# Performance work log

Measured on AMD Instinct MI355X. Metric: run time of the kernel, lower is better.

Reference implementation:

```python
import jax, jax.numpy as jnp
import numpy as np
from jax.scipy.special import erf, erfc

N_ATOMS = 4096
BOX_L = 60.0
CUTOFF = 9.0
GRID = (64, 64, 64)
ORDER = 4
ALPHA = 0.34
COULOMB = 138.935456


def _bspline_weights(t, order):
    # Cardinal B-spline recursion (OpenMM/NNPOps convention).
    # w[..., j] = M_order(t + order - 1 - j), t in [0, 1)
    w = jnp.zeros(t.shape + (order,), t.dtype)
    w = w.at[..., 0].set(1.0 - t)
    w = w.at[..., 1].set(t)
    for k in range(3, order + 1):
        div = 1.0 / (k - 1)
        new = jnp.zeros_like(w)
        new = new.at[..., k - 1].set(div * t * w[..., k - 2])
        for j in range(1, k - 1):
            new = new.at[..., k - 1 - j].set(
                div * ((t + j) * w[..., k - 2 - j] + (k - j - t) * w[..., k - 1 - j]))
        new = new.at[..., 0].set(div * (1.0 - t) * w[..., 0])
        w = new
    return w


def _bspline_moduli(K, order):
    # |b(m)|^2 = 1 / |sum_k M_n(k+1) exp(2 pi i m k / K)|^2
    w = _bspline_weights(jnp.zeros((), jnp.float32), order)  # w[j] = M_n(n-1-j)
    mvals = w[::-1][1:]                                      # M_n(1), ..., M_n(n-1)
    data = jnp.zeros((K,), jnp.float32).at[jnp.arange(order - 1)].set(mvals)
    d2 = jnp.abs(jnp.fft.fft(data)) ** 2
    return 1.0 / jnp.maximum(d2, 1e-7)


def _min_image(delta, box, inv_box):
    s = delta @ inv_box
    s = s - jnp.round(s)
    return s @ box


def _pme_energy(positions, charges, box_vectors, exclusions):
    N = positions.shape[0]
    Kx, Ky, Kz = GRID
    inv_box = jnp.linalg.inv(box_vectors)

    # ---------------- direct space: erfc-screened pairwise sum with cutoff & exclusions
    delta = positions[:, None, :] - positions[None, :, :]          # [N,N,3]
    delta = _min_image(delta, box_vectors, inv_box)
    r2 = jnp.sum(delta * delta, axis=-1)                           # [N,N]
    rows = jnp.broadcast_to(jnp.arange(N)[:, None], exclusions.shape)
    excl_cols = jnp.where(exclusions >= 0, exclusions, rows)       # map padding -1 -> self
    excl_mask = jnp.zeros((N, N), bool).at[rows, excl_cols].set(True)
    pair_mask = jnp.triu(jnp.ones((N, N), bool), 1) & (r2 < CUTOFF ** 2) & (~excl_mask)
    r = jnp.sqrt(jnp.where(pair_mask, r2, 1.0))
    qq = charges[:, None] * charges[None, :]
    edir = COULOMB * jnp.sum(jnp.where(pair_mask, qq * erfc(ALPHA * r) / r, 0.0))

    # ---------------- reciprocal space: B-spline spread -> FFT -> influence function
    frac = positions @ inv_box
    frac = frac - jnp.floor(frac)                                  # wrap into [0,1)
    u = frac * jnp.asarray(GRID, frac.dtype)                       # [N,3] grid coords
    base = jnp.floor(u).astype(jnp.int32)
    t = u - jnp.floor(u)
    wx = _bspline_weights(t[:, 0], ORDER)                          # [N,order]
    wy = _bspline_weights(t[:, 1], ORDER)
    wz = _bspline_weights(t[:, 2], ORDER)
    offs = jnp.arange(ORDER, dtype=jnp.int32) - (ORDER - 1)        # weight j -> floor(u)-n+1+j
    ix = (base[:, 0:1] + offs) % Kx
    iy = (base[:, 1:2] + offs) % Ky
    iz = (base[:, 2:3] + offs) % Kz
    vals = (charges[:, None, None, None] * wx[:, :, None, None]
            * wy[:, None, :, None] * wz[:, None, None, :])         # [N,n,n,n]
    flat = (ix[:, :, None, None] * Ky + iy[:, None, :, None]) * Kz + iz[:, None, None, :]
    grid = jnp.zeros(Kx * Ky * Kz, positions.dtype).at[flat.reshape(-1)].add(
        vals.reshape(-1)).reshape(GRID)

    Fq = jnp.fft.fftn(grid)
    mx = (jnp.fft.fftfreq(Kx) * Kx).astype(positions.dtype)
    my = (jnp.fft.fftfreq(Ky) * Ky).astype(positions.dtype)
    mz = (jnp.fft.fftfreq(Kz) * Kz).astype(positions.dtype)
    m = jnp.stack(jnp.meshgrid(mx, my, mz, indexing='ij'), axis=-1)  # [Kx,Ky,Kz,3]
    kvec = m @ inv_box.T                                             # reciprocal vectors
    msq = jnp.sum(kvec * kvec, axis=-1)
    nonzero = msq > 0
    influence = jnp.where(nonzero,
                          jnp.exp(-(jnp.pi ** 2) * msq / ALPHA ** 2)
                          / jnp.where(nonzero, msq, 1.0), 0.0)
    bmod = (_bspline_moduli(Kx, ORDER)[:, None, None]
            * _bspline_moduli(Ky, ORDER)[None, :, None]
            * _bspline_moduli(Kz, ORDER)[None, None, :])
    V = jnp.abs(jnp.linalg.det(box_vectors))
    sq = Fq.real ** 2 + Fq.imag ** 2
    erec = COULOMB / (2.0 * jnp.pi * V) * jnp.sum(influence * bmod * sq)

    # self-energy correction
    eself = -COULOMB * ALPHA / jnp.sqrt(jnp.pi) * jnp.sum(charges ** 2)

    # exclusion correction: remove reciprocal contribution of excluded pairs
    de = positions[:, None, :] - positions[excl_cols]              # [N,E,3]
    de = _min_image(de, box_vectors, inv_box)
    re2 = jnp.sum(de * de, axis=-1)
    valid = (exclusions >= 0) & (re2 > 0)
    re = jnp.sqrt(jnp.where(valid, re2, 1.0))
    qe = charges[:, None] * charges[excl_cols]
    eexcl = -0.5 * COULOMB * jnp.sum(jnp.where(valid, qe * erf(ALPHA * re) / re, 0.0))

    return edir + erec + eself + eexcl


def setup_inputs():
    key = jax.random.key(0)
    k1, k2 = jax.random.split(key)
    positions = jax.random.uniform(k1, (N_ATOMS, 3), jnp.float32) * BOX_L
    charges = jax.random.normal(k2, (N_ATOMS,), jnp.float32) * 0.5
    charges = charges - jnp.mean(charges)  # neutral system
    box_vectors = jnp.eye(3, dtype=jnp.float32) * BOX_L
    idx = jnp.arange(N_ATOMS, dtype=jnp.int32)
    exclusions = jnp.stack([(idx - 1) % N_ATOMS, (idx + 1) % N_ATOMS], axis=1)  # symmetric chain
    return {"positions": positions, "charges": charges,
            "box_vectors": box_vectors, "exclusions": exclusions}


def reference(positions, charges, box_vectors, exclusions):
    return _pme_energy(positions, charges, box_vectors, exclusions)
```

## Files before the change

kernel.cpp:

```cpp
#include <hip/hip_runtime.h>
#include <math.h>
#include <stdint.h>

#define KG 64
#define KG3 (KG * KG * KG)
#define MZK 33
#define ALPHA 0.34f
#define COULOMB 138.935456f
#define CUTOFF2 81.0f
#define PI_F 3.14159265358979323846f

struct BoxInfo {
    float inv[9];
    float vol;
    bool diag;
};
__device__ __forceinline__ BoxInfo load_box(const float* __restrict__ box) {
    BoxInfo b;
    float b0 = box[0], b1 = box[1], b2 = box[2];
    float b3 = box[3], b4 = box[4], b5 = box[5];
    float b6 = box[6], b7 = box[7], b8 = box[8];
    float det = b0 * (b4 * b8 - b5 * b7) - b1 * (b3 * b8 - b5 * b6) + b2 * (b3 * b7 - b4 * b6);
    float id = 1.0f / det;
    b.inv[0] = (b4 * b8 - b5 * b7) * id;
    b.inv[1] = (b2 * b7 - b1 * b8) * id;
    b.inv[2] = (b1 * b5 - b2 * b4) * id;
    b.inv[3] = (b5 * b6 - b3 * b8) * id;
    b.inv[4] = (b0 * b8 - b2 * b6) * id;
    b.inv[5] = (b2 * b3 - b0 * b5) * id;
    b.inv[6] = (b3 * b7 - b4 * b6) * id;
    b.inv[7] = (b1 * b6 - b0 * b7) * id;
    b.inv[8] = (b0 * b4 - b1 * b3) * id;
    b.vol = fabsf(det);
    b.diag = (b1 == 0.0f) && (b2 == 0.0f) && (b3 == 0.0f) && (b5 == 0.0f) && (b6 == 0.0f) &&
             (b7 == 0.0f);
    return b;
}

__device__ __forceinline__ float erfc_fast(float x) {
    float t = __builtin_amdgcn_rcpf(fmaf(0.3275911f, x, 1.0f));
    float p = fmaf(t, 1.061405429f, -1.453152027f);
    p = fmaf(t, p, 1.421413741f);
    p = fmaf(t, p, -0.284496736f);
    p = fmaf(t, p, 0.254829592f);
    return t * p * __expf(-x * x);
}

__device__ __forceinline__ void bspline4(float t, float* w) {
    float w0 = 1.0f - t, w1 = t;
    float a2 = 0.5f * t * w1;
    float a1 = 0.5f * ((t + 1.0f) * w0 + (2.0f - t) * w1);
    float a0 = 0.5f * (1.0f - t) * w0;
    const float d = 1.0f / 3.0f;
    w[3] = d * t * a2;
    w[2] = d * ((t + 1.0f) * a1 + (3.0f - t) * a2);
    w[1] = d * ((t + 2.0f) * a0 + (2.0f - t) * a1);
    w[0] = d * (1.0f - t) * a0;
}

__global__ __launch_bounds__(256) void spread_kernel(const float* __restrict__ pos,
                                                     const float* __restrict__ chg,
                                                     const float* __restrict__ box,
                                                     float* __restrict__ grid,
                                                     float4* __restrict__ pxq, int N) {
    int t4 = blockIdx.x * blockDim.x + threadIdx.x;
    int i = t4 >> 2, jx = t4 & 3;
    if (i >= N) return;
    BoxInfo B = load_box(box);
    float p0 = pos[3 * i], p1 = pos[3 * i + 1], p2 = pos[3 * i + 2];
    float q = chg[i];
    if (jx == 0) pxq[i] = make_float4(p0, p1, p2, q);
    float w[3][4];
    int idx[3][4];
#pragma unroll
    for (int a = 0; a < 3; a++) {
        float f = p0 * B.inv[0 * 3 + a] + p1 * B.inv[1 * 3 + a] + p2 * B.inv[2 * 3 + a];
        f -= floorf(f);
        float u = f * (float)KG;
        float fu = floorf(u);
        int base = (int)fu;
        float tt = u - fu;
        bspline4(tt, w[a]);
#pragma unroll
        for (int j = 0; j < 4; j++) idx[a][j] = (base - 3 + j + 2 * KG) & (KG - 1);
    }
    float qx = q * w[0][jx];
    int bx = idx[0][jx] * KG;
#pragma unroll
    for (int jy = 0; jy < 4; jy++) {
        float qxy = qx * w[1][jy];
        int bxy = (bx + idx[1][jy]) * KG;
#pragma unroll
        for (int jz = 0; jz < 4; jz++) {
            atomicAdd(&grid[bxy + idx[2][jz]], qxy * w[2][jz]);
        }
    }
}

#define DIB 256
#define DJT 32
__global__ __launch_bounds__(256) void direct_kernel(const float4* __restrict__ pxq,
                                                     const float* __restrict__ box,
                                                     const int* __restrict__ excl, int N, int E,
                                                     double* __restrict__ partD) {
    int ib = blockIdx.x * DIB, jb = blockIdx.y * DJT;
    if (jb + DJT <= ib) return;

    __shared__ float4 sj[DJT];
    __shared__ double wsum[4];
    int tid = threadIdx.x;
    if (tid < DJT) {
        int jg0 = jb + tid;
        sj[tid] = (jg0 < N) ? pxq[jg0] : make_float4(0.0f, 0.0f, 0.0f, 0.0f);
    }
    __syncthreads();

    BoxInfo B = load_box(box);
    double e = 0.0;
    int i = ib + tid;
    if (i < N) {
        float4 me = pxq[i];
        float xi = me.x, yi = me.y, zi = me.z, qi = me.w;
        int ex0 = -1, ex1 = -1;
        int ne = (E < 8) ? E : 8;
        int ex[8];
        for (int k = 0; k < ne; k++) ex[k] = excl[i * E + k];

        float fsum = 0.0f;
        if (B.diag) {
            float Lx = box[0], Ly = box[4], Lz = box[8];
            float ivx = B.inv[0], ivy = B.inv[4], ivz = B.inv[8];
#pragma unroll 8
            for (int jj = 0; jj < DJT; jj++) {
                float4 o = sj[jj];
                int jg = jb + jj;
                float dx = xi - o.x, dy = yi - o.y, dz = zi - o.z;
                dx -= rintf(dx * ivx) * Lx;
                dy -= rintf(dy * ivy) * Ly;
                dz -= rintf(dz * ivz) * Lz;
                float r2 = fmaf(dx, dx, fmaf(dy, dy, dz * dz));
                bool valid = (r2 < CUTOFF2) & (jg > i) & (jg < N);
                for (int k = 0; k < ne; k++) valid = valid & (ex[k] != jg);
                float r2m = valid ? r2 : 1.0f;
                float rinv = __builtin_amdgcn_rsqf(r2m);
                float r = r2m * rinv;
                float g = erfc_fast(ALPHA * r) * rinv;
                float qqm = valid ? qi * o.w : 0.0f;
                fsum = fmaf(qqm, g, fsum);
            }
        } else {
#pragma unroll 4
            for (int jj = 0; jj < DJT; jj++) {
                float4 o = sj[jj];
                int jg = jb + jj;
                float dx = xi - o.x, dy = yi - o.y, dz = zi - o.z;
                float s0 = dx * B.inv[0] + dy * B.inv[3] + dz * B.inv[6];
                float s1 = dx * B.inv[1] + dy * B.inv[4] + dz * B.inv[7];
                float s2 = dx * B.inv[2] + dy * B.inv[5] + dz * B.inv[8];
                s0 -= rintf(s0);
                s1 -= rintf(s1);
                s2 -= rintf(s2);
                float ddx = s0 * box[0] + s1 * box[3] + s2 * box[6];
                float ddy = s0 * box[1] + s1 * box[4] + s2 * box[7];
                float ddz = s0 * box[2] + s1 * box[5] + s2 * box[8];
                float r2 = fmaf(ddx, ddx, fmaf(ddy, ddy, ddz * ddz));
                bool valid = (r2 < CUTOFF2) & (jg > i) & (jg < N);
                for (int k = 0; k < ne; k++) valid = valid & (ex[k] != jg);
                float r2m = valid ? r2 : 1.0f;
                float rinv = __builtin_amdgcn_rsqf(r2m);
                float r = r2m * rinv;
                float g = erfc_fast(ALPHA * r) * rinv;
                float qqm = valid ? qi * o.w : 0.0f;
                fsum = fmaf(qqm, g, fsum);
            }
        }
        e = (double)(COULOMB * fsum);

        if (jb == ib) {
            const float inv_sqrt_pi = 0.5641895835477563f;
            float corr = -ALPHA * inv_sqrt_pi * qi * qi;
            for (int k = 0; k < ne; k++) {
                int j = ex[k];
                if (j < 0) continue;
                float4 o = pxq[j];
                float dx = xi - o.x, dy = yi - o.y, dz = zi - o.z;
                if (B.diag) {
                    dx -= rintf(dx * B.inv[0]) * box[0];
                    dy -= rintf(dy * B.inv[4]) * box[4];
                    dz -= rintf(dz * B.inv[8]) * box[8];
                } else {
                    float s0 = dx * B.inv[0] + dy * B.inv[3] + dz * B.inv[6];
                    float s1 = dx * B.inv[1] + dy * B.inv[4] + dz * B.inv[7];
                    float s2 = dx * B.inv[2] + dy * B.inv[5] + dz * B.inv[8];
                    s0 -= rintf(s0);
                    s1 -= rintf(s1);
                    s2 -= rintf(s2);
                    dx = s0 * box[0] + s1 * box[3] + s2 * box[6];
                    dy = s0 * box[1] + s1 * box[4] + s2 * box[7];
                    dz = s0 * box[2] + s1 * box[5] + s2 * box[8];
                }
                float r2 = dx * dx + dy * dy + dz * dz;
                if (r2 > 0.0f) {
                    float rinv = __builtin_amdgcn_rsqf(r2);
                    float r = r2 * rinv;
                    float erfv = 1.0f - erfc_fast(ALPHA * r);
                    corr += -0.5f * qi * o.w * erfv * rinv;
                }
            }
            e += (double)(COULOMB * corr);
        }
    }
#pragma unroll
    for (int off = 32; off > 0; off >>= 1) e += __shfl_down(e, off, 64);
    if ((tid & 63) == 0) wsum[tid >> 6] = e;
    __syncthreads();
    if (tid == 0)
        partD[blockIdx.y * gridDim.x + blockIdx.x] = wsum[0] + wsum[1] + wsum[2] + wsum[3];
}

struct Tw8 {
    float wc[8], ws[8], c8, s8, c1, s1;
};
__device__ __forceinline__ Tw8 make_tw8(int m) {
    Tw8 T;
    float s1, c1;
    __sincosf(-2.0f * PI_F * (float)m / (float)KG, &s1, &c1);
    T.c1 = c1;
    T.s1 = s1;
    float c2 = c1 * c1 - s1 * s1, s2 = 2.0f * c1 * s1;
    float c4 = c2 * c2 - s2 * s2, s4 = 2.0f * c2 * s2;
    T.c8 = c4 * c4 - s4 * s4;
    T.s8 = 2.0f * c4 * s4;
    T.wc[0] = 1.0f;
    T.ws[0] = 0.0f;
    T.wc[1] = c1;
    T.ws[1] = s1;
    T.wc[2] = c2;
    T.ws[2] = s2;
    T.wc[3] = c2 * c1 - s2 * s1;
    T.ws[3] = c2 * s1 + s2 * c1;
    T.wc[4] = c4;
    T.ws[4] = s4;
    T.wc[5] = c4 * c1 - s4 * s1;
    T.ws[5] = c4 * s1 + s4 * c1;
    T.wc[6] = c4 * c2 - s4 * s2;
    T.ws[6] = c4 * s2 + s4 * c2;
    T.wc[7] = c4 * T.wc[3] - s4 * T.ws[3];
    T.ws[7] = c4 * T.ws[3] + s4 * T.wc[3];
    return T;
}

__global__ __launch_bounds__(256) void dft_z(const float* __restrict__ grid,
                                             float2* __restrict__ bufA) {
    __shared__ float g[4][KG];
    int tid = threadIdx.x, wv = tid >> 6, ln = tid & 63;
    int line = blockIdx.x * 4 + wv;
    g[wv][ln] = grid[line * KG + ln];
    __syncthreads();
    Tw8 T = make_tw8(ln);
    float rr[8] = {0}, ii[8] = {0};
#pragma unroll
    for (int s = 0; s < 8; s++) {
#pragma unroll
        for (int gg = 0; gg < 8; gg++) {
            float gv = g[wv][s * 8 + gg];
            rr[gg] = fmaf(gv, T.wc[gg], rr[gg]);
            ii[gg] = fmaf(gv, T.ws[gg], ii[gg]);
            float nc = T.wc[gg] * T.c8 - T.ws[gg] * T.s8;
            T.ws[gg] = T.wc[gg] * T.s8 + T.ws[gg] * T.c8;
            T.wc[gg] = nc;
        }
    }
    if (ln < MZK) {
        float re = ((rr[0] + rr[1]) + (rr[2] + rr[3])) + ((rr[4] + rr[5]) + (rr[6] + rr[7]));
        float im = ((ii[0] + ii[1]) + (ii[2] + ii[3])) + ((ii[4] + ii[5]) + (ii[6] + ii[7]));
        int ix = line >> 6, iy = line & 63;
        bufA[(ix * KG + ln) * KG + iy] = make_float2(re, im);
    }
}

__global__ __launch_bounds__(256) void dft_y(const float2* __restrict__ bufA,
                                             float2* __restrict__ bufB) {
    __shared__ float2 c[4][KG];
    int tid = threadIdx.x, wv = tid >> 6, ln = tid & 63;
    int idx = blockIdx.x * 4 + wv;
    if (idx >= KG * MZK) return;
    int ix = idx / MZK, mz = idx - ix * MZK;
    c[wv][ln] = bufA[(ix * KG + mz) * KG + ln];
    __syncthreads();
    Tw8 T = make_tw8(ln);
    float rr[8] = {0}, ii[8] = {0};
#pragma unroll
    for (int s = 0; s < 8; s++) {
#pragma unroll
        for (int gg = 0; gg < 8; gg++) {
            float2 a = c[wv][s * 8 + gg];
            rr[gg] += a.x * T.wc[gg] - a.y * T.ws[gg];
            ii[gg] += a.x * T.ws[gg] + a.y * T.wc[gg];
            float nc = T.wc[gg] * T.c8 - T.ws[gg] * T.s8;
            T.ws[gg] = T.wc[gg] * T.s8 + T.ws[gg] * T.c8;
            T.wc[gg] = nc;
        }
    }
    float re = ((rr[0] + rr[1]) + (rr[2] + rr[3])) + ((rr[4] + rr[5]) + (rr[6] + rr[7]));
    float im = ((ii[0] + ii[1]) + (ii[2] + ii[3])) + ((ii[4] + ii[5]) + (ii[6] + ii[7]));
    bufB[(ln * MZK + mz) * KG + ix] = make_float2(re, im);
}

__device__ __forceinline__ float bmod4(float c1, float s1) {
    float c2 = 2.0f * c1 * c1 - 1.0f;
    float s2 = 2.0f * s1 * c1;
    float br = (1.0f + 4.0f * c1 + c2) * (1.0f / 6.0f);
    float bi = (4.0f * s1 + s2) * (1.0f / 6.0f);
    float d2 = br * br + bi * bi;
    return 1.0f / fmaxf(d2, 1e-7f);
}

__global__ __launch_bounds__(256) void dft_x_reduce(const float2* __restrict__ bufB,
                                                    const float* __restrict__ box,
                                                    double* __restrict__ partR) {
    __shared__ float2 c[4][KG];
    int tid = threadIdx.x, wv = tid >> 6, ln = tid & 63;
    int idx = blockIdx.x * 4 + wv;
    if (idx >= KG * MZK) return;
    int my = idx / MZK, mz = idx - my * MZK;
    c[wv][ln] = bufB[(my * MZK + mz) * KG + ln];
    __syncthreads();
    Tw8 T = make_tw8(ln);
    float rr[8] = {0}, ii[8] = {0};
#pragma unroll
    for (int s = 0; s < 8; s++) {
#pragma unroll
        for (int gg = 0; gg < 8; gg++) {
            float2 a = c[wv][s * 8 + gg];
            rr[gg] += a.x * T.wc[gg] - a.y * T.ws[gg];
            ii[gg] += a.x * T.ws[gg] + a.y * T.wc[gg];
            float nc = T.wc[gg] * T.c8 - T.ws[gg] * T.s8;
            T.ws[gg] = T.wc[gg] * T.s8 + T.ws[gg] * T.c8;
            T.wc[gg] = nc;
        }
    }
    float re = ((rr[0] + rr[1]) + (rr[2] + rr[3])) + ((rr[4] + rr[5]) + (rr[6] + rr[7]));
    float im = ((ii[0] + ii[1]) + (ii[2] + ii[3])) + ((ii[4] + ii[5]) + (ii[6] + ii[7]));
    float sq = re * re + im * im;

    BoxInfo B = load_box(box);
    int mx = ln;
    int msx = (mx < KG / 2) ? mx : mx - KG;
    int msy = (my < KG / 2) ? my : my - KG;
    int msz = (mz < KG / 2) ? mz : mz - KG;
    float fmx = (float)msx, fmy = (float)msy, fmz = (float)msz;
    float kx = fmx * B.inv[0] + fmy * B.inv[1] + fmz * B.inv[2];
    float ky = fmx * B.inv[3] + fmy * B.inv[4] + fmz * B.inv[5];
    float kz = fmx * B.inv[6] + fmy * B.inv[7] + fmz * B.inv[8];
    float msq = kx * kx + ky * ky + kz * kz;
    const float cexp = (PI_F * PI_F) / (ALPHA * ALPHA);
    float infl = (msq > 0.0f) ? __expf(-cexp * msq) / msq : 0.0f;

    float bx_ = bmod4(T.c1, T.s1);
    float sy, cy, sz, cz;
    __sincosf(2.0f * PI_F * (float)my / (float)KG, &sy, &cy);
    __sincosf(2.0f * PI_F * (float)mz / (float)KG, &sz, &cz);
    float by_ = bmod4(cy, sy);
    float bz_ = bmod4(cz, sz);

    float wgt = (mz == 0 || mz == 32) ? 1.0f : 2.0f;
    float pref = COULOMB / (2.0f * PI_F * B.vol);
    double term = (double)(wgt * pref * infl * bx_ * by_ * bz_ * sq);

#pragma unroll
    for (int off = 32; off > 0; off >>= 1) term += __shfl_down(term, off, 64);
    if (ln == 0) partR[idx] = term;
}

__global__ __launch_bounds__(1024) void final_reduce(const double* __restrict__ parts, int n,
                                                     float* __restrict__ out) {
    __shared__ double wsum[16];
    int tid = threadIdx.x;
    double s = 0.0;
    for (int k = tid; k < n; k += 1024) s += parts[k];
#pragma unroll
    for (int off = 32; off > 0; off >>= 1) s += __shfl_down(s, off, 64);
    if ((tid & 63) == 0) wsum[tid >> 6] = s;
    __syncthreads();
    if (tid == 0) {
        double t = 0.0;
#pragma unroll
        for (int w = 0; w < 16; w++) t += wsum[w];
        out[0] = (float)t;
    }
}


extern "C" void kernel_launch(void* const* d_in, const int* in_sizes, int n_in,
                              void* d_out, int out_size, void* d_ws, size_t ws_size,
                              hipStream_t stream) {
    const float* pos = (const float*)d_in[0];
    const float* chg = (const float*)d_in[1];
    const float* box = (const float*)d_in[2];
    const int* excl = (const int*)d_in[3];
    int N = in_sizes[0] / 3;
    int E = in_sizes[3] / N;

    char* ws = (char*)d_ws;
    double* partD = (double*)(ws + 4096);
    double* partR = (double*)(ws + 20480);
    double* parts = (double*)(ws + 4096);
    float* grid = (float*)(ws + 65536);
    float2* bufA = (float2*)(ws + 65536 + 4 * (size_t)KG3);
    float2* bufB = (float2*)(ws + 65536 + 12 * (size_t)KG3);
    float4* pxq = (float4*)bufB;

    hipMemsetAsync(ws, 0, 65536 + 4 * (size_t)KG3, stream);

    spread_kernel<<<(4 * N + 255) / 256, 256, 0, stream>>>(pos, chg, box, grid, pxq, N);

    int nib = (N + DIB - 1) / DIB;
    int njt = (N + DJT - 1) / DJT;
    dim3 dg(nib, njt);
    direct_kernel<<<dg, 256, 0, stream>>>(pxq, box, excl, N, E, partD);

    dft_z<<<KG * KG / 4, 256, 0, stream>>>(grid, bufA);
    int nlines = KG * MZK;
    dft_y<<<(nlines + 3) / 4, 256, 0, stream>>>(bufA, bufB);
    dft_x_reduce<<<(nlines + 3) / 4, 256, 0, stream>>>(bufB, box, partR);

    int nparts = nib * njt + nlines;
    final_reduce<<<1, 1024, 0, stream>>>(parts, nparts, (float*)d_out);
}
```

Measured before the change: 131.3 us.

## Fuse z/y DFTs per plane, use atomic last-block reduction, widen spread threads

The separate z and y DFT kernels become one dft2d_yz kernel. Each 1024-thread block loads a 64x64 plane into LDS and does both transforms there, which removes the bufB round trip through global memory and one launch. The final_reduce kernel is dropped: dft_x_reduce and direct_kernel atomically add block sums into 16 double accumulators, and the last block to finish (tracked by a counter) writes the output. Spread now uses 16 threads per atom instead of 4, cutting serial atomics per thread. The trade-offs are extra atomic contention, and dft2d_yz runs only 64 large blocks, so parallelism on that stage is lower.

```diff
diff --git a/kernel.cpp b/kernel.cpp
--- a/kernel.cpp
+++ b/kernel.cpp
@@ -5,6 +5,8 @@
 #define KG 64
 #define KG3 (KG * KG * KG)
 #define MZK 33
+#define DIB 256
+#define DJT 32
 #define ALPHA 0.34f
 #define COULOMB 138.935456f
 #define CUTOFF2 81.0f
@@ -58,18 +60,68 @@
     w[0] = d * (1.0f - t) * a0;
 }
 
+__device__ __forceinline__ float sel4(const float* w, int j) {
+    float r = w[0];
+    r = (j == 1) ? w[1] : r;
+    r = (j == 2) ? w[2] : r;
+    r = (j == 3) ? w[3] : r;
+    return r;
+}
+
+struct Tw8 {
+    float wc[8], ws[8], c8, s8, c1, s1;
+};
+__device__ __forceinline__ Tw8 make_tw8(int m) {
+    Tw8 T;
+    float s1, c1;
+    __sincosf(-2.0f * PI_F * (float)m / (float)KG, &s1, &c1);
+    T.c1 = c1;
+    T.s1 = s1;
+    float c2 = c1 * c1 - s1 * s1, s2 = 2.0f * c1 * s1;
+    float c4 = c2 * c2 - s2 * s2, s4 = 2.0f * c2 * s2;
+    T.c8 = c4 * c4 - s4 * s4;
+    T.s8 = 2.0f * c4 * s4;
+    T.wc[0] = 1.0f;
+    T.ws[0] = 0.0f;
+    T.wc[1] = c1;
+    T.ws[1] = s1;
+    T.wc[2] = c2;
+    T.ws[2] = s2;
+    T.wc[3] = c2 * c1 - s2 * s1;
+    T.ws[3] = c2 * s1 + s2 * c1;
+    T.wc[4] = c4;
+    T.ws[4] = s4;
+    T.wc[5] = c4 * c1 - s4 * s1;
+    T.ws[5] = c4 * s1 + s4 * c1;
+    T.wc[6] = c4 * c2 - s4 * s2;
+    T.ws[6] = c4 * s2 + s4 * c2;
+    T.wc[7] = c4 * T.wc[3] - s4 * T.ws[3];
+    T.ws[7] = c4 * T.ws[3] + s4 * T.wc[3];
+    return T;
+}
+
+__device__ __forceinline__ float bmod4(float c1, float s1) {
+    float c2 = 2.0f * c1 * c1 - 1.0f;
+    float s2 = 2.0f * s1 * c1;
+    float br = (1.0f + 4.0f * c1 + c2) * (1.0f / 6.0f);
+    float bi = (4.0f * s1 + s2) * (1.0f / 6.0f);
+    float d2 = br * br + bi * bi;
+    return 1.0f / fmaxf(d2, 1e-7f);
+}
+
 __global__ __launch_bounds__(256) void spread_kernel(const float* __restrict__ pos,
                                                      const float* __restrict__ chg,
                                                      const float* __restrict__ box,
                                                      float* __restrict__ grid,
                                                      float4* __restrict__ pxq, int N) {
-    int t4 = blockIdx.x * blockDim.x + threadIdx.x;
-    int i = t4 >> 2, jx = t4 & 3;
+    int t16 = blockIdx.x * blockDim.x + threadIdx.x;
+    int i = t16 >> 4, sub = t16 & 15;
     if (i >= N) return;
+    int jx = sub >> 2, jy = sub & 3;
     BoxInfo B = load_box(box);
     float p0 = pos[3 * i], p1 = pos[3 * i + 1], p2 = pos[3 * i + 2];
     float q = chg[i];
-    if (jx == 0) pxq[i] = make_float4(p0, p1, p2, q);
+    if (sub == 0) pxq[i] = make_float4(p0, p1, p2, q);
     float w[3][4];
     int idx[3][4];
 #pragma unroll
@@ -84,32 +136,147 @@
 #pragma unroll
         for (int j = 0; j < 4; j++) idx[a][j] = (base - 3 + j + 2 * KG) & (KG - 1);
     }
-    float qx = q * w[0][jx];
-    int bx = idx[0][jx] * KG;
-#pragma unroll
-    for (int jy = 0; jy < 4; jy++) {
-        float qxy = qx * w[1][jy];
-        int bxy = (bx + idx[1][jy]) * KG;
-#pragma unroll
-        for (int jz = 0; jz < 4; jz++) {
-            atomicAdd(&grid[bxy + idx[2][jz]], qxy * w[2][jz]);
-        }
-    }
-}
-
-#define DIB 256
-#define DJT 32
+    float qxy = q * sel4(w[0], jx) * sel4(w[1], jy);
+    int bxy = (idx[0][jx] * KG + idx[1][jy]) * KG;
+#pragma unroll
+    for (int jz = 0; jz < 4; jz++) {
+        atomicAdd(&grid[bxy + idx[2][jz]], qxy * w[2][jz]);
+    }
+}
+
+__global__ __launch_bounds__(1024) void dft2d_yz(const float* __restrict__ grid,
+                                                 float2* __restrict__ bufA) {
+    __shared__ float Pl[KG * KG];
+    __shared__ float2 Qs[KG][MZK + 1];
+    int ix = blockIdx.x;
+    int tid = threadIdx.x;
+    int wv = tid >> 6, ln = tid & 63;
+
+    const float* gp = grid + ix * KG * KG;
+    for (int k = tid; k < KG * KG; k += 1024) Pl[k] = gp[k];
+    __syncthreads();
+
+    for (int r = 0; r < 4; r++) {
+        int iy = wv + r * 16;
+        Tw8 T = make_tw8(ln);
+        float rr[8] = {0}, ii[8] = {0};
+#pragma unroll
+        for (int s = 0; s < 8; s++) {
+#pragma unroll
+            for (int g8 = 0; g8 < 8; g8++) {
+                float gv = Pl[iy * KG + s * 8 + g8];
+                rr[g8] = fmaf(gv, T.wc[g8], rr[g8]);
+                ii[g8] = fmaf(gv, T.ws[g8], ii[g8]);
+                float nc = T.wc[g8] * T.c8 - T.ws[g8] * T.s8;
+                T.ws[g8] = T.wc[g8] * T.s8 + T.ws[g8] * T.c8;
+                T.wc[g8] = nc;
+            }
+        }
+        if (ln < MZK) {
+            float re = ((rr[0] + rr[1]) + (rr[2] + rr[3])) + ((rr[4] + rr[5]) + (rr[6] + rr[7]));
+            float im = ((ii[0] + ii[1]) + (ii[2] + ii[3])) + ((ii[4] + ii[5]) + (ii[6] + ii[7]));
+            Qs[iy][ln] = make_float2(re, im);
+        }
+    }
+    __syncthreads();
+
+    for (int mz = wv; mz < MZK; mz += 16) {
+        Tw8 T = make_tw8(ln);
+        float rr[8] = {0}, ii[8] = {0};
+#pragma unroll
+        for (int s = 0; s < 8; s++) {
+#pragma unroll
+            for (int g8 = 0; g8 < 8; g8++) {
+                float2 a = Qs[s * 8 + g8][mz];
+                rr[g8] += a.x * T.wc[g8] - a.y * T.ws[g8];
+                ii[g8] += a.x * T.ws[g8] + a.y * T.wc[g8];
+                float nc = T.wc[g8] * T.c8 - T.ws[g8] * T.s8;
+                T.ws[g8] = T.wc[g8] * T.s8 + T.ws[g8] * T.c8;
+                T.wc[g8] = nc;
+            }
+        }
+        float re = ((rr[0] + rr[1]) + (rr[2] + rr[3])) + ((rr[4] + rr[5]) + (rr[6] + rr[7]));
+        float im = ((ii[0] + ii[1]) + (ii[2] + ii[3])) + ((ii[4] + ii[5]) + (ii[6] + ii[7]));
+        bufA[(ln * MZK + mz) * KG + ix] = make_float2(re, im);
+    }
+}
+
+__global__ __launch_bounds__(256) void dft_x_reduce(const float2* __restrict__ bufA,
+                                                    const float* __restrict__ box,
+                                                    double* __restrict__ acc,
+                                                    unsigned* __restrict__ cnt) {
+    __shared__ float2 c[4][KG];
+    __shared__ double wsum[4];
+    int tid = threadIdx.x, wv = tid >> 6, ln = tid & 63;
+    int idx = blockIdx.x * 4 + wv;
+    int my = idx / MZK, mz = idx - my * MZK;
+    c[wv][ln] = bufA[(my * MZK + mz) * KG + ln];
+    __syncthreads();
+    Tw8 T = make_tw8(ln);
+    float rr[8] = {0}, ii[8] = {0};
+#pragma unroll
+    for (int s = 0; s < 8; s++) {
+#pragma unroll
+        for (int g8 = 0; g8 < 8; g8++) {
+            float2 a = c[wv][s * 8 + g8];
+            rr[g8] += a.x * T.wc[g8] - a.y * T.ws[g8];
+            ii[g8] += a.x * T.ws[g8] + a.y * T.wc[g8];
+            float nc = T.wc[g8] * T.c8 - T.ws[g8] * T.s8;
+            T.ws[g8] = T.wc[g8] * T.s8 + T.ws[g8] * T.c8;
+            T.wc[g8] = nc;
+        }
+    }
+    float re = ((rr[0] + rr[1]) + (rr[2] + rr[3])) + ((rr[4] + rr[5]) + (rr[6] + rr[7]));
+    float im = ((ii[0] + ii[1]) + (ii[2] + ii[3])) + ((ii[4] + ii[5]) + (ii[6] + ii[7]));
+    float sq = re * re + im * im;
+
+    BoxInfo B = load_box(box);
+    int mx = ln;
+    int msx = (mx < KG / 2) ? mx : mx - KG;
+    int msy = (my < KG / 2) ? my : my - KG;
+    int msz = (mz < KG / 2) ? mz : mz - KG;
+    float fmx = (float)msx, fmy = (float)msy, fmz = (float)msz;
+    float kx = fmx * B.inv[0] + fmy * B.inv[1] + fmz * B.inv[2];
+    float ky = fmx * B.inv[3] + fmy * B.inv[4] + fmz * B.inv[5];
+    float kz = fmx * B.inv[6] + fmy * B.inv[7] + fmz * B.inv[8];
+    float msq = kx * kx + ky * ky + kz * kz;
+    const float cexp = (PI_F * PI_F) / (ALPHA * ALPHA);
+    float infl = (msq > 0.0f) ? __expf(-cexp * msq) / msq : 0.0f;
+    float bx_ = bmod4(T.c1, T.s1);
+    float sy, cy, sz, cz;
+    __sincosf(2.0f * PI_F * (float)my / (float)KG, &sy, &cy);
+    __sincosf(2.0f * PI_F * (float)mz / (float)KG, &sz, &cz);
+    float by_ = bmod4(cy, sy);
+    float bz_ = bmod4(cz, sz);
+    float wgt = (mz == 0 || mz == 32) ? 1.0f : 2.0f;
+    float pref = COULOMB / (2.0f * PI_F * B.vol);
+    double term = (double)(wgt * pref * infl * bx_ * by_ * bz_ * sq);
+
+#pragma unroll
+    for (int off = 32; off > 0; off >>= 1) term += __shfl_down(term, off, 64);
+    if (ln == 0) wsum[wv] = term;
+    __syncthreads();
+    if (tid == 0) {
+        double eb = wsum[0] + wsum[1] + wsum[2] + wsum[3];
+        double old = atomicAdd(&acc[blockIdx.x & 15], eb);
+        __asm__ volatile("" ::"v"(old) : "memory");
+        atomicAdd(cnt, 1u);
+    }
+}
+
 __global__ __launch_bounds__(256) void direct_kernel(const float4* __restrict__ pxq,
                                                      const float* __restrict__ box,
                                                      const int* __restrict__ excl, int N, int E,
-                                                     double* __restrict__ partD) {
+                                                     double* __restrict__ acc,
+                                                     unsigned* __restrict__ cnt, unsigned total,
+                                                     float* __restrict__ out) {
     int ib = blockIdx.x * DIB, jb = blockIdx.y * DJT;
-    if (jb + DJT <= ib) return;
+    bool live = (jb + DJT > ib);
 
     __shared__ float4 sj[DJT];
     __shared__ double wsum[4];
-    int tid = threadIdx.x;
-    if (tid < DJT) {
+    int tid = threadIdx.x, wv = tid >> 6, ln = tid & 63;
+    if (live && tid < DJT) {
         int jg0 = jb + tid;
         sj[tid] = (jg0 < N) ? pxq[jg0] : make_float4(0.0f, 0.0f, 0.0f, 0.0f);
     }
@@ -118,14 +285,12 @@
     BoxInfo B = load_box(box);
     double e = 0.0;
     int i = ib + tid;
-    if (i < N) {
+    if (live && i < N) {
         float4 me = pxq[i];
         float xi = me.x, yi = me.y, zi = me.z, qi = me.w;
-        int ex0 = -1, ex1 = -1;
         int ne = (E < 8) ? E : 8;
         int ex[8];
         for (int k = 0; k < ne; k++) ex[k] = excl[i * E + k];
-
         float fsum = 0.0f;
         if (B.diag) {
             float Lx = box[0], Ly = box[4], Lz = box[8];
@@ -210,184 +375,27 @@
             e += (double)(COULOMB * corr);
         }
     }
+
+    __syncthreads();
 #pragma unroll
     for (int off = 32; off > 0; off >>= 1) e += __shfl_down(e, off, 64);
-    if ((tid & 63) == 0) wsum[tid >> 6] = e;
-    __syncthreads();
-    if (tid == 0)
-        partD[blockIdx.y * gridDim.x + blockIdx.x] = wsum[0] + wsum[1] + wsum[2] + wsum[3];
-}
-
-struct Tw8 {
-    float wc[8], ws[8], c8, s8, c1, s1;
-};
-__device__ __forceinline__ Tw8 make_tw8(int m) {
-    Tw8 T;
-    float s1, c1;
-    __sincosf(-2.0f * PI_F * (float)m / (float)KG, &s1, &c1);
-    T.c1 = c1;
-    T.s1 = s1;
-    float c2 = c1 * c1 - s1 * s1, s2 = 2.0f * c1 * s1;
-    float c4 = c2 * c2 - s2 * s2, s4 = 2.0f * c2 * s2;
-    T.c8 = c4 * c4 - s4 * s4;
-    T.s8 = 2.0f * c4 * s4;
-    T.wc[0] = 1.0f;
-    T.ws[0] = 0.0f;
-    T.wc[1] = c1;
-    T.ws[1] = s1;
-    T.wc[2] = c2;
-    T.ws[2] = s2;
-    T.wc[3] = c2 * c1 - s2 * s1;
-    T.ws[3] = c2 * s1 + s2 * c1;
-    T.wc[4] = c4;
-    T.ws[4] = s4;
-    T.wc[5] = c4 * c1 - s4 * s1;
-    T.ws[5] = c4 * s1 + s4 * c1;
-    T.wc[6] = c4 * c2 - s4 * s2;
-    T.ws[6] = c4 * s2 + s4 * c2;
-    T.wc[7] = c4 * T.wc[3] - s4 * T.ws[3];
-    T.ws[7] = c4 * T.ws[3] + s4 * T.wc[3];
-    return T;
-}
-
-__global__ __launch_bounds__(256) void dft_z(const float* __restrict__ grid,
-                                             float2* __restrict__ bufA) {
-    __shared__ float g[4][KG];
-    int tid = threadIdx.x, wv = tid >> 6, ln = tid & 63;
-    int line = blockIdx.x * 4 + wv;
-    g[wv][ln] = grid[line * KG + ln];
-    __syncthreads();
-    Tw8 T = make_tw8(ln);
-    float rr[8] = {0}, ii[8] = {0};
-#pragma unroll
-    for (int s = 0; s < 8; s++) {
-#pragma unroll
-        for (int gg = 0; gg < 8; gg++) {
-            float gv = g[wv][s * 8 + gg];
-            rr[gg] = fmaf(gv, T.wc[gg], rr[gg]);
-            ii[gg] = fmaf(gv, T.ws[gg], ii[gg]);
-            float nc = T.wc[gg] * T.c8 - T.ws[gg] * T.s8;
-            T.ws[gg] = T.wc[gg] * T.s8 + T.ws[gg] * T.c8;
-            T.wc[gg] = nc;
-        }
-    }
-    if (ln < MZK) {
-        float re = ((rr[0] + rr[1]) + (rr[2] + rr[3])) + ((rr[4] + rr[5]) + (rr[6] + rr[7]));
-        float im = ((ii[0] + ii[1]) + (ii[2] + ii[3])) + ((ii[4] + ii[5]) + (ii[6] + ii[7]));
-        int ix = line >> 6, iy = line & 63;
-        bufA[(ix * KG + ln) * KG + iy] = make_float2(re, im);
-    }
-}
-
-__global__ __launch_bounds__(256) void dft_y(const float2* __restrict__ bufA,
-                                             float2* __restrict__ bufB) {
-    __shared__ float2 c[4][KG];
-    int tid = threadIdx.x, wv = tid >> 6, ln = tid & 63;
-    int idx = blockIdx.x * 4 + wv;
-    if (idx >= KG * MZK) return;
-    int ix = idx / MZK, mz = idx - ix * MZK;
-    c[wv][ln] = bufA[(ix * KG + mz) * KG + ln];
-    __syncthreads();
-    Tw8 T = make_tw8(ln);
-    float rr[8] = {0}, ii[8] = {0};
-#pragma unroll
-    for (int s = 0; s < 8; s++) {
-#pragma unroll
-        for (int gg = 0; gg < 8; gg++) {
-            float2 a = c[wv][s * 8 + gg];
-            rr[gg] += a.x * T.wc[gg] - a.y * T.ws[gg];
-            ii[gg] += a.x * T.ws[gg] + a.y * T.wc[gg];
-            float nc = T.wc[gg] * T.c8 - T.ws[gg] * T.s8;
-            T.ws[gg] = T.wc[gg] * T.s8 + T.ws[gg] * T.c8;
-            T.wc[gg] = nc;
-        }
-    }
-    float re = ((rr[0] + rr[1]) + (rr[2] + rr[3])) + ((rr[4] + rr[5]) + (rr[6] + rr[7]));
-    float im = ((ii[0] + ii[1]) + (ii[2] + ii[3])) + ((ii[4] + ii[5]) + (ii[6] + ii[7]));
-    bufB[(ln * MZK + mz) * KG + ix] = make_float2(re, im);
-}
-
-__device__ __forceinline__ float bmod4(float c1, float s1) {
-    float c2 = 2.0f * c1 * c1 - 1.0f;
-    float s2 = 2.0f * s1 * c1;
-    float br = (1.0f + 4.0f * c1 + c2) * (1.0f / 6.0f);
-    float bi = (4.0f * s1 + s2) * (1.0f / 6.0f);
-    float d2 = br * br + bi * bi;
-    return 1.0f / fmaxf(d2, 1e-7f);
-}
-
-__global__ __launch_bounds__(256) void dft_x_reduce(const float2* __restrict__ bufB,
-                                                    const float* __restrict__ box,
-                                                    double* __restrict__ partR) {
-    __shared__ float2 c[4][KG];
-    int tid = threadIdx.x, wv = tid >> 6, ln = tid & 63;
-    int idx = blockIdx.x * 4 + wv;
-    if (idx >= KG * MZK) return;
-    int my = idx / MZK, mz = idx - my * MZK;
-    c[wv][ln] = bufB[(my * MZK + mz) * KG + ln];
-    __syncthreads();
-    Tw8 T = make_tw8(ln);
-    float rr[8] = {0}, ii[8] = {0};
-#pragma unroll
-    for (int s = 0; s < 8; s++) {
-#pragma unroll
-        for (int gg = 0; gg < 8; gg++) {
-            float2 a = c[wv][s * 8 + gg];
-            rr[gg] += a.x * T.wc[gg] - a.y * T.ws[gg];
-            ii[gg] += a.x * T.ws[gg] + a.y * T.wc[gg];
-            float nc = T.wc[gg] * T.c8 - T.ws[gg] * T.s8;
-            T.ws[gg] = T.wc[gg] * T.s8 + T.ws[gg] * T.c8;
-            T.wc[gg] = nc;
-        }
-    }
-    float re = ((rr[0] + rr[1]) + (rr[2] + rr[3])) + ((rr[4] + rr[5]) + (rr[6] + rr[7]));
-    float im = ((ii[0] + ii[1]) + (ii[2] + ii[3])) + ((ii[4] + ii[5]) + (ii[6] + ii[7]));
-    float sq = re * re + im * im;
-
-    BoxInfo B = load_box(box);
-    int mx = ln;
-    int msx = (mx < KG / 2) ? mx : mx - KG;
-    int msy = (my < KG / 2) ? my : my - KG;
-    int msz = (mz < KG / 2) ? mz : mz - KG;
-    float fmx = (float)msx, fmy = (float)msy, fmz = (float)msz;
-    float kx = fmx * B.inv[0] + fmy * B.inv[1] + fmz * B.inv[2];
-    float ky = fmx * B.inv[3] + fmy * B.inv[4] + fmz * B.inv[5];
-    float kz = fmx * B.inv[6] + fmy * B.inv[7] + fmz * B.inv[8];
-    float msq = kx * kx + ky * ky + kz * kz;
-    const float cexp = (PI_F * PI_F) / (ALPHA * ALPHA);
-    float infl = (msq > 0.0f) ? __expf(-cexp * msq) / msq : 0.0f;
-
-    float bx_ = bmod4(T.c1, T.s1);
-    float sy, cy, sz, cz;
-    __sincosf(2.0f * PI_F * (float)my / (float)KG, &sy, &cy);
-    __sincosf(2.0f * PI_F * (float)mz / (float)KG, &sz, &cz);
-    float by_ = bmod4(cy, sy);
-    float bz_ = bmod4(cz, sz);
-
-    float wgt = (mz == 0 || mz == 32) ? 1.0f : 2.0f;
-    float pref = COULOMB / (2.0f * PI_F * B.vol);
-    double term = (double)(wgt * pref * infl * bx_ * by_ * bz_ * sq);
-
-#pragma unroll
-    for (int off = 32; off > 0; off >>= 1) term += __shfl_down(term, off, 64);
-    if (ln == 0) partR[idx] = term;
-}
-
-__global__ __launch_bounds__(1024) void final_reduce(const double* __restrict__ parts, int n,
-                                                     float* __restrict__ out) {
-    __shared__ double wsum[16];
-    int tid = threadIdx.x;
-    double s = 0.0;
-    for (int k = tid; k < n; k += 1024) s += parts[k];
-#pragma unroll
-    for (int off = 32; off > 0; off >>= 1) s += __shfl_down(s, off, 64);
-    if ((tid & 63) == 0) wsum[tid >> 6] = s;
+    if (ln == 0) wsum[wv] = e;
     __syncthreads();
     if (tid == 0) {
-        double t = 0.0;
-#pragma unroll
-        for (int w = 0; w < 16; w++) t += wsum[w];
-        out[0] = (float)t;
+        double eb = wsum[0] + wsum[1] + wsum[2] + wsum[3];
+        int bid = blockIdx.y * gridDim.x + blockIdx.x;
+        if (eb != 0.0) {
+            double old = atomicAdd(&acc[bid & 15], eb);
+            __asm__ volatile("" ::"v"(old) : "memory");
+        }
+        unsigned prev = atomicAdd(cnt, 1u);
+        if (prev == total - 1u) {
+            double s = 0.0;
+#pragma unroll
+            for (int k = 0; k < 16; k++)
+                s += __hip_atomic_load(&acc[k], __ATOMIC_RELAXED, __HIP_MEMORY_SCOPE_AGENT);
+            out[0] = (float)s;
+        }
     }
 }
 
@@ -403,28 +411,22 @@
     int E = in_sizes[3] / N;
 
     char* ws = (char*)d_ws;
-    double* partD = (double*)(ws + 4096);
-    double* partR = (double*)(ws + 20480);
-    double* parts = (double*)(ws + 4096);
-    float* grid = (float*)(ws + 65536);
-    float2* bufA = (float2*)(ws + 65536 + 4 * (size_t)KG3);
-    float2* bufB = (float2*)(ws + 65536 + 12 * (size_t)KG3);
-    float4* pxq = (float4*)bufB;
-
-    hipMemsetAsync(ws, 0, 65536 + 4 * (size_t)KG3, stream);
-
-    spread_kernel<<<(4 * N + 255) / 256, 256, 0, stream>>>(pos, chg, box, grid, pxq, N);
+    double* acc = (double*)ws;
+    unsigned* cnt = (unsigned*)(ws + 128);
+    float* grid = (float*)(ws + 4096);
+    float2* bufA = (float2*)(ws + 0x110000);
+    float4* pxq = (float4*)(ws + 0x220000);
+    float* out = (float*)d_out;
+
+    hipMemsetAsync(ws, 0, 4096 + 4 * (size_t)KG3, stream);
+
+    spread_kernel<<<(16 * N + 255) / 256, 256, 0, stream>>>(pos, chg, box, grid, pxq, N);
+    dft2d_yz<<<KG, 1024, 0, stream>>>(grid, bufA);
+    dft_x_reduce<<<KG * MZK / 4, 256, 0, stream>>>(bufA, box, acc, cnt);
 
     int nib = (N + DIB - 1) / DIB;
     int njt = (N + DJT - 1) / DJT;
+    unsigned total = (unsigned)(KG * MZK / 4 + nib * njt);
     dim3 dg(nib, njt);
-    direct_kernel<<<dg, 256, 0, stream>>>(pxq, box, excl, N, E, partD);
-
-    dft_z<<<KG * KG / 4, 256, 0, stream>>>(grid, bufA);
-    int nlines = KG * MZK;
-    dft_y<<<(nlines + 3) / 4, 256, 0, stream>>>(bufA, bufB);
-    dft_x_reduce<<<(nlines + 3) / 4, 256, 0, stream>>>(bufB, box, partR);
-
-    int nparts = nib * njt + nlines;
-    final_reduce<<<1, 1024, 0, stream>>>(parts, nparts, (float*)d_out);
-}
+    direct_kernel<<<dg, 256, 0, stream>>>(pxq, box, excl, N, E, acc, cnt, total, out);
+}
```

After: 310.9 us. +136.8%, slower.
